# Optimization experiments

Measured on AMD Instinct MI355X. Metric: run time of the kernel, lower is better.

## Reference

```python
import jax, jax.numpy as jnp
import numpy as np

N_NODES = 50000
N_EDGES = 800000
N_GRAPHS = 64
D_IN, D_HID, D_OUT = 128, 128, 64


def setup_inputs() -> dict:
    key = jax.random.key(0)
    ks = jax.random.split(key, 9)
    s = 0.05
    return {
        "x": jax.random.normal(ks[0], (N_NODES, D_IN), jnp.float32),
        "edge_index": jax.random.randint(ks[1], (2, N_EDGES), 0, N_NODES, dtype=jnp.int64),
        "batch": jnp.sort(jax.random.randint(ks[2], (N_NODES,), 0, N_GRAPHS, dtype=jnp.int64)),
        "W1": jax.random.normal(ks[3], (D_IN, D_HID), jnp.float32) * s,
        "b1": jnp.zeros((D_HID,), jnp.float32),
        "W2": jax.random.normal(ks[4], (D_HID, D_HID), jnp.float32) * s,
        "b2": jnp.zeros((D_HID,), jnp.float32),
        "W3": jax.random.normal(ks[5], (D_HID, D_OUT), jnp.float32) * s,
        "b3": jnp.zeros((D_OUT,), jnp.float32),
    }


def _gcn_conv(x, W, b, src, dst, dinv, n_nodes):
    # PyG GCNConv: h = X W; out = sum_{j->i} norm_ij h_j + self-loop term + b
    h = x @ W
    norm_e = dinv[src] * dinv[dst]                      # [E]
    agg = jax.ops.segment_sum(norm_e[:, None] * h[src], dst, num_segments=n_nodes)
    agg = agg + (dinv * dinv)[:, None] * h              # self-loop (norm = dinv_i^2)
    return agg + b


def reference(x, edge_index, batch, W1, b1, W2, b2, W3, b3):
    n_nodes = x.shape[0]
    src, dst = edge_index[0], edge_index[1]
    # symmetric normalization with self-loops: deg_i = in_degree_i + 1
    deg = jax.ops.segment_sum(jnp.ones_like(dst, dtype=x.dtype), dst, num_segments=n_nodes) + 1.0
    dinv = jax.lax.rsqrt(deg)

    h = jax.nn.relu(_gcn_conv(x, W1, b1, src, dst, dinv, n_nodes))
    h = jax.nn.relu(_gcn_conv(h, W2, b2, src, dst, dinv, n_nodes))
    h = _gcn_conv(h, W3, b3, src, dst, dinv, n_nodes)

    # global_mean_pool over graph id
    sums = jax.ops.segment_sum(h, batch, num_segments=N_GRAPHS)
    counts = jax.ops.segment_sum(jnp.ones((n_nodes,), h.dtype), batch, num_segments=N_GRAPHS)
    return sums / jnp.maximum(counts, 1.0)[:, None]
```

## Files before the change

kernel.cpp:

```cpp
#include <hip/hip_runtime.h>

#define NN 50000
#define NE 800000
#define NG 64

typedef short short8 __attribute__((ext_vector_type(8)));
typedef float f32x4 __attribute__((ext_vector_type(4)));

__device__ __forceinline__ unsigned short f2bf(float f) {
    unsigned int u = __float_as_uint(f);
    u = (u + 0x7FFFu + ((u >> 16) & 1u)) >> 16;
    return (unsigned short)u;
}
__device__ __forceinline__ float bf2f(unsigned short h) {
    return __uint_as_float((unsigned int)h << 16);
}

__global__ __launch_bounds__(256) void k_deg(const int* __restrict__ dst, int* __restrict__ degcnt) {
    int e = blockIdx.x * 256 + threadIdx.x;
    if (e < NE) atomicAdd(&degcnt[dst[e]], 1);
}

__global__ __launch_bounds__(256) void k_dinv(const int* __restrict__ degcnt, float* __restrict__ dinv) {
    int i = blockIdx.x * 256 + threadIdx.x;
    if (i < NN) dinv[i] = (float)(1.0 / sqrt((double)degcnt[i] + 1.0));
}

__global__ __launch_bounds__(1024) void k_scan1(const int* __restrict__ cnt, int* __restrict__ row_ptr,
                                                int* __restrict__ blk_sums) {
    __shared__ int s[1024];
    const int tid = threadIdx.x;
    const int i = blockIdx.x * 1024 + tid;
    int v = (i < NN) ? cnt[i] : 0;
    s[tid] = v;
    __syncthreads();
    for (int off = 1; off < 1024; off <<= 1) {
        int t = (tid >= off) ? s[tid - off] : 0;
        __syncthreads();
        s[tid] += t;
        __syncthreads();
    }
    if (i < NN) row_ptr[i] = s[tid] - v;
    if (tid == 1023) blk_sums[blockIdx.x] = s[1023];
}

__global__ __launch_bounds__(64) void k_scan2(int* __restrict__ blk_sums, int nb) {
    int l = threadIdx.x;
    int v = (l < nb) ? blk_sums[l] : 0;
    int incl = v;
    for (int off = 1; off < 64; off <<= 1) {
        int t = __shfl_up(incl, off, 64);
        if (l >= off) incl += t;
    }
    if (l < nb) blk_sums[l] = incl - v;
}

__global__ __launch_bounds__(1024) void k_scan3(int* __restrict__ row_ptr, const int* __restrict__ blk_sums) {
    int i = blockIdx.x * 1024 + threadIdx.x;
    if (i < NN) row_ptr[i] += blk_sums[blockIdx.x];
    if (i == 0) row_ptr[NN] = NE;
}

__global__ __launch_bounds__(256) void k_fill(const int* __restrict__ ei, const int* __restrict__ row_ptr,
                                              int* __restrict__ cursor, int* __restrict__ csr_src) {
    int e = blockIdx.x * 256 + threadIdx.x;
    if (e >= NE) return;
    int s = ei[e];
    int d = ei[NE + e];
    int pos = row_ptr[d] + atomicAdd(&cursor[d], 1);
    csr_src[pos] = s;
}

template <int DO>
__global__ __launch_bounds__(256) void k_gemm_mfma(const float* __restrict__ A, const float* __restrict__ W,
                                                   unsigned short* __restrict__ C, int M) {
    constexpr int NT = DO / 16;
    constexpr int LDK = 136;
    __shared__ __align__(16) unsigned short As[64 * LDK];
    __shared__ __align__(16) unsigned short Wt[DO * LDK];
    const int tid = threadIdx.x;
    const int row0 = blockIdx.x * 64;

    for (int task = tid; task < 64 * (DO / 4); task += 256) {
        const int k0 = (task / (DO / 4)) * 2;
        const int n4 = (task % (DO / 4)) * 4;
        const float4 wa = *(const float4*)&W[(size_t)k0 * DO + n4];
        const float4 wb = *(const float4*)&W[(size_t)(k0 + 1) * DO + n4];
        const float pa[4] = {wa.x, wa.y, wa.z, wa.w};
        const float pb[4] = {wb.x, wb.y, wb.z, wb.w};
#pragma unroll
        for (int i = 0; i < 4; ++i) {
            const unsigned int pk = (unsigned int)f2bf(pa[i]) | ((unsigned int)f2bf(pb[i]) << 16);
            *(unsigned int*)&Wt[(n4 + i) * LDK + k0] = pk;
        }
    }
    {
        const int r = tid >> 2;
        const int ks = (tid & 3) * 32;
        const int grow = row0 + r;
#pragma unroll
        for (int q = 0; q < 8; ++q) {
            float4 v = make_float4(0.f, 0.f, 0.f, 0.f);
            if (grow < M) v = *(const float4*)&A[(size_t)grow * 128 + ks + q * 4];
            const unsigned long long pk =
                (unsigned long long)f2bf(v.x) | ((unsigned long long)f2bf(v.y) << 16) |
                ((unsigned long long)f2bf(v.z) << 32) | ((unsigned long long)f2bf(v.w) << 48);
            *(unsigned long long*)&As[r * LDK + ks + q * 4] = pk;
        }
    }
    __syncthreads();

    const int l = tid & 63;
    const int w = tid >> 6;
    const int lr = l & 15;
    const int lg = l >> 4;
    f32x4 acc[NT];
#pragma unroll
    for (int nt = 0; nt < NT; ++nt) acc[nt] = (f32x4){0.f, 0.f, 0.f, 0.f};

#pragma unroll
    for (int kk = 0; kk < 128; kk += 32) {
        const short8 af = *(const short8*)&As[(w * 16 + lr) * LDK + kk + lg * 8];
#pragma unroll
        for (int nt = 0; nt < NT; ++nt) {
            const short8 bfv = *(const short8*)&Wt[(nt * 16 + lr) * LDK + kk + lg * 8];
            acc[nt] = __builtin_amdgcn_mfma_f32_16x16x32_bf16(af, bfv, acc[nt], 0, 0, 0);
        }
    }

#pragma unroll
    for (int nt = 0; nt < NT; ++nt) {
#pragma unroll
        for (int r = 0; r < 4; ++r) {
            const int grow = row0 + w * 16 + lg * 4 + r;
            if (grow < M) C[(size_t)grow * DO + nt * 16 + lr] = f2bf(acc[nt][r]);
        }
    }
}

template <int D, bool RELU>
__global__ __launch_bounds__(256) void k_agg(const unsigned short* __restrict__ T, const float* __restrict__ bias,
                                             const float* __restrict__ dinv, const int* __restrict__ row_ptr,
                                             const int* __restrict__ csr_src,
                                             float* __restrict__ out) {
    constexpr int G = D / 4;
    constexpr int NPB = 256 / G;
    const int tid = threadIdx.x;
    const int lane = tid % G;
    const int grp = tid / G;
    const int n = blockIdx.x * NPB + grp;
    if (n >= NN) return;

    const float di_n = dinv[n];
    double a0 = 0.0, a1 = 0.0, a2 = 0.0, a3 = 0.0;
    const int beg = row_ptr[n];
    const int end = row_ptr[n + 1];
    int e = beg;
    for (; e + 4 <= end; e += 4) {
        const int s0 = csr_src[e + 0], s1 = csr_src[e + 1], s2 = csr_src[e + 2], s3 = csr_src[e + 3];
        const float w0 = dinv[s0] * di_n, w1 = dinv[s1] * di_n, w2 = dinv[s2] * di_n, w3 = dinv[s3] * di_n;
        const ushort4 v0 = *(const ushort4*)&T[(size_t)s0 * D + lane * 4];
        const ushort4 v1 = *(const ushort4*)&T[(size_t)s1 * D + lane * 4];
        const ushort4 v2 = *(const ushort4*)&T[(size_t)s2 * D + lane * 4];
        const ushort4 v3 = *(const ushort4*)&T[(size_t)s3 * D + lane * 4];
        a0 += (double)w0 * bf2f(v0.x) + (double)w1 * bf2f(v1.x) + (double)w2 * bf2f(v2.x) + (double)w3 * bf2f(v3.x);
        a1 += (double)w0 * bf2f(v0.y) + (double)w1 * bf2f(v1.y) + (double)w2 * bf2f(v2.y) + (double)w3 * bf2f(v3.y);
        a2 += (double)w0 * bf2f(v0.z) + (double)w1 * bf2f(v1.z) + (double)w2 * bf2f(v2.z) + (double)w3 * bf2f(v3.z);
        a3 += (double)w0 * bf2f(v0.w) + (double)w1 * bf2f(v1.w) + (double)w2 * bf2f(v2.w) + (double)w3 * bf2f(v3.w);
    }
    for (; e < end; ++e) {
        const int s = csr_src[e];
        const float w = dinv[s] * di_n;
        const ushort4 v = *(const ushort4*)&T[(size_t)s * D + lane * 4];
        a0 += (double)w * bf2f(v.x);
        a1 += (double)w * bf2f(v.y);
        a2 += (double)w * bf2f(v.z);
        a3 += (double)w * bf2f(v.w);
    }
    {
        const double w = (double)di_n * (double)di_n;
        const ushort4 v = *(const ushort4*)&T[(size_t)n * D + lane * 4];
        a0 += w * bf2f(v.x);
        a1 += w * bf2f(v.y);
        a2 += w * bf2f(v.z);
        a3 += w * bf2f(v.w);
    }
    const float4 b = *(const float4*)&bias[lane * 4];
    a0 += b.x; a1 += b.y; a2 += b.z; a3 += b.w;
    float4 r;
    r.x = (float)a0; r.y = (float)a1; r.z = (float)a2; r.w = (float)a3;
    if (RELU) {
        r.x = fmaxf(r.x, 0.f);
        r.y = fmaxf(r.y, 0.f);
        r.z = fmaxf(r.z, 0.f);
        r.w = fmaxf(r.w, 0.f);
    }
    *(float4*)&out[(size_t)n * D + lane * 4] = r;
}

__global__ __launch_bounds__(256) void k_pool(const float* __restrict__ h, const int* __restrict__ batch,
                                              double* __restrict__ sums, int* __restrict__ cnts) {
    const int NB = 256;
    const int n0 = blockIdx.x * NB;
    const int d = threadIdx.x & 63;
    const int sub = threadIdx.x >> 6;
    double acc = 0.0;
    int cnt = 0;
    int cur = -1;
    for (int i = sub; i < NB; i += 4) {
        int n = n0 + i;
        if (n >= NN) break;
        int g = batch[n];
        if (g != cur) {
            if (cur >= 0) {
                atomicAdd(&sums[cur * 64 + d], acc);
                if (d == 0) atomicAdd(&cnts[cur], cnt);
            }
            cur = g;
            acc = 0.0;
            cnt = 0;
        }
        acc += (double)h[(size_t)n * 64 + d];
        cnt++;
    }
    if (cur >= 0) {
        atomicAdd(&sums[cur * 64 + d], acc);
        if (d == 0) atomicAdd(&cnts[cur], cnt);
    }
}

__global__ __launch_bounds__(256) void k_final(const double* __restrict__ sums, const int* __restrict__ cnts,
                                               float* __restrict__ out) {
    int i = blockIdx.x * 256 + threadIdx.x;
    if (i >= NG * 64) return;
    int g = i >> 6;
    double c = (double)max(cnts[g], 1);
    out[i] = (float)(sums[i] / c);
}

extern "C" void kernel_launch(void* const* d_in, const int* in_sizes, int n_in,
                              void* d_out, int out_size, void* d_ws, size_t ws_size,
                              hipStream_t stream) {
    (void)in_sizes; (void)n_in; (void)out_size; (void)ws_size;
    const float* x     = (const float*)d_in[0];
    const int*   ei    = (const int*)d_in[1];
    const int*   batch = (const int*)d_in[2];
    const float* W1    = (const float*)d_in[3];
    const float* b1    = (const float*)d_in[4];
    const float* W2    = (const float*)d_in[5];
    const float* b2    = (const float*)d_in[6];
    const float* W3    = (const float*)d_in[7];
    const float* b3    = (const float*)d_in[8];
    float* out = (float*)d_out;

    char* w = (char*)d_ws;
    char*  zbase = w;
    int*    degcnt = (int*)w;           w += (size_t)NN * 4;
    int*    cursor = (int*)w;           w += (size_t)NN * 4;
    double* psums  = (double*)w;        w += (size_t)NG * 64 * 8;
    int*    pcnts  = (int*)w;           w += 256;
    size_t zbytes = (size_t)(w - zbase);
    float* dinv     = (float*)w;        w += (size_t)NN * 4;
    int*   row_ptr  = (int*)w;          w += (size_t)(NN + 4) * 4;
    int*   blk_sums = (int*)w;          w += 64 * 4;
    int*   csr_src  = (int*)w;          w += (size_t)NE * 4;
    unsigned short* bufT = (unsigned short*)w;  w += (size_t)NN * 128 * 2;
    float* bufA = (float*)w;            w += (size_t)NN * 128 * 4;

    hipMemsetAsync(zbase, 0, zbytes, stream);

    const int nb_scan = (NN + 1023) / 1024;
    k_deg<<<(NE + 255) / 256, 256, 0, stream>>>(ei + NE, degcnt);
    k_dinv<<<(NN + 255) / 256, 256, 0, stream>>>(degcnt, dinv);
    k_scan1<<<nb_scan, 1024, 0, stream>>>(degcnt, row_ptr, blk_sums);
    k_scan2<<<1, 64, 0, stream>>>(blk_sums, nb_scan);
    k_scan3<<<nb_scan, 1024, 0, stream>>>(row_ptr, blk_sums);
    k_fill<<<(NE + 255) / 256, 256, 0, stream>>>(ei, row_ptr, cursor, csr_src);

    const int gemm_grid = (NN + 63) / 64;
    k_gemm_mfma<128><<<gemm_grid, 256, 0, stream>>>(x, W1, bufT, NN);
    k_agg<128, true><<<(NN + 7) / 8, 256, 0, stream>>>(bufT, b1, dinv, row_ptr, csr_src, bufA);
    k_gemm_mfma<128><<<gemm_grid, 256, 0, stream>>>(bufA, W2, bufT, NN);
    k_agg<128, true><<<(NN + 7) / 8, 256, 0, stream>>>(bufT, b2, dinv, row_ptr, csr_src, bufA);
    k_gemm_mfma<64><<<gemm_grid, 256, 0, stream>>>(bufA, W3, bufT, NN);
    k_agg<64, false><<<(NN + 15) / 16, 256, 0, stream>>>(bufT, b3, dinv, row_ptr, csr_src, bufA);
    k_pool<<<(NN + 255) / 256, 256, 0, stream>>>(bufA, batch, psums, pcnts);
    k_final<<<(NG * 64 + 255) / 256, 256, 0, stream>>>(psums, pcnts, out);
}
```

Before: 297.2 us.

## Build CSR with per-chunk LDS histograms instead of global atomics

Replaces the global atomic degree count and the atomic cursor fill with a two-pass counting sort. Per-chunk shared-memory histograms record each edge's rank within its chunk, and a column scan produces per-chunk offsets, so the fill needs no atomics. The aim is to remove global atomic contention and the zeroed cursor buffer. In exchange it adds two kernels and a 64×50000 uint16 offset table that must be written and read back.

Result: faster. 252.8 us (-14.9%).

```diff
diff --git a/kernel.cpp b/kernel.cpp
--- a/kernel.cpp
+++ b/kernel.cpp
@@ -3,6 +3,9 @@
 #define NN 50000
 #define NE 800000
 #define NG 64
+#define NCHUNK 64
+#define CHUNK 12500
+#define HALF 25000
 
 typedef short short8 __attribute__((ext_vector_type(8)));
 typedef float f32x4 __attribute__((ext_vector_type(4)));
@@ -16,9 +19,41 @@
     return __uint_as_float((unsigned int)h << 16);
 }
 
-__global__ __launch_bounds__(256) void k_deg(const int* __restrict__ dst, int* __restrict__ degcnt) {
-    int e = blockIdx.x * 256 + threadIdx.x;
-    if (e < NE) atomicAdd(&degcnt[dst[e]], 1);
+__global__ __launch_bounds__(1024) void k_hist(const int* __restrict__ ei,
+                                               unsigned short* __restrict__ rank,
+                                               unsigned short* __restrict__ percnt) {
+    __shared__ unsigned int cnt[HALF / 2];
+    const int b = blockIdx.x;
+    const int dbase = blockIdx.y * HALF;
+    const int tid = threadIdx.x;
+    for (int i = tid; i < HALF / 2; i += 1024) cnt[i] = 0;
+    __syncthreads();
+    const int e0 = b * CHUNK;
+    for (int i = tid; i < CHUNK; i += 1024) {
+        const int d = ei[NE + e0 + i];
+        const int local = d - dbase;
+        if ((unsigned)local < (unsigned)HALF) {
+            const unsigned int old = atomicAdd(&cnt[local >> 1], 1u << ((local & 1) * 16));
+            rank[e0 + i] = (unsigned short)((old >> ((local & 1) * 16)) & 0xFFFFu);
+        }
+    }
+    __syncthreads();
+    unsigned int* dst = (unsigned int*)&percnt[(size_t)b * NN + dbase];
+    for (int i = tid; i < HALF / 2; i += 1024) dst[i] = cnt[i];
+}
+
+__global__ __launch_bounds__(256) void k_colscan(unsigned short* __restrict__ percnt,
+                                                 int* __restrict__ degcnt) {
+    const int d = blockIdx.x * 256 + threadIdx.x;
+    if (d >= NN) return;
+    int acc = 0;
+#pragma unroll 8
+    for (int b = 0; b < NCHUNK; ++b) {
+        const int c = percnt[(size_t)b * NN + d];
+        percnt[(size_t)b * NN + d] = (unsigned short)acc;
+        acc += c;
+    }
+    degcnt[d] = acc;
 }
 
 __global__ __launch_bounds__(256) void k_dinv(const int* __restrict__ degcnt, float* __restrict__ dinv) {
@@ -61,13 +96,16 @@
     if (i == 0) row_ptr[NN] = NE;
 }
 
-__global__ __launch_bounds__(256) void k_fill(const int* __restrict__ ei, const int* __restrict__ row_ptr,
-                                              int* __restrict__ cursor, int* __restrict__ csr_src) {
-    int e = blockIdx.x * 256 + threadIdx.x;
+__global__ __launch_bounds__(256) void k_fill3(const int* __restrict__ ei, const int* __restrict__ row_ptr,
+                                               const unsigned short* __restrict__ rank,
+                                               const unsigned short* __restrict__ offs,
+                                               int* __restrict__ csr_src) {
+    const int e = blockIdx.x * 256 + threadIdx.x;
     if (e >= NE) return;
-    int s = ei[e];
-    int d = ei[NE + e];
-    int pos = row_ptr[d] + atomicAdd(&cursor[d], 1);
+    const int s = ei[e];
+    const int d = ei[NE + e];
+    const int b = e / CHUNK;
+    const int pos = row_ptr[d] + (int)offs[(size_t)b * NN + d] + (int)rank[e];
     csr_src[pos] = s;
 }
 
@@ -255,27 +293,29 @@
 
     char* w = (char*)d_ws;
     char*  zbase = w;
-    int*    degcnt = (int*)w;           w += (size_t)NN * 4;
-    int*    cursor = (int*)w;           w += (size_t)NN * 4;
     double* psums  = (double*)w;        w += (size_t)NG * 64 * 8;
     int*    pcnts  = (int*)w;           w += 256;
     size_t zbytes = (size_t)(w - zbase);
-    float* dinv     = (float*)w;        w += (size_t)NN * 4;
-    int*   row_ptr  = (int*)w;          w += (size_t)(NN + 4) * 4;
-    int*   blk_sums = (int*)w;          w += 64 * 4;
-    int*   csr_src  = (int*)w;          w += (size_t)NE * 4;
+    int*    degcnt = (int*)w;           w += (size_t)NN * 4;
+    float*  dinv   = (float*)w;         w += (size_t)NN * 4;
+    int*    row_ptr = (int*)w;          w += (size_t)(NN + 4) * 4;
+    int*    blk_sums = (int*)w;         w += 64 * 4;
+    unsigned short* rank   = (unsigned short*)w;  w += (size_t)NE * 2;
+    unsigned short* percnt = (unsigned short*)w;  w += (size_t)NCHUNK * NN * 2;
+    int*    csr_src = (int*)w;          w += (size_t)NE * 4;
     unsigned short* bufT = (unsigned short*)w;  w += (size_t)NN * 128 * 2;
     float* bufA = (float*)w;            w += (size_t)NN * 128 * 4;
 
     hipMemsetAsync(zbase, 0, zbytes, stream);
 
+    k_hist<<<dim3(NCHUNK, 2), 1024, 0, stream>>>(ei, rank, percnt);
+    k_colscan<<<(NN + 255) / 256, 256, 0, stream>>>(percnt, degcnt);
+    k_dinv<<<(NN + 255) / 256, 256, 0, stream>>>(degcnt, dinv);
     const int nb_scan = (NN + 1023) / 1024;
-    k_deg<<<(NE + 255) / 256, 256, 0, stream>>>(ei + NE, degcnt);
-    k_dinv<<<(NN + 255) / 256, 256, 0, stream>>>(degcnt, dinv);
     k_scan1<<<nb_scan, 1024, 0, stream>>>(degcnt, row_ptr, blk_sums);
     k_scan2<<<1, 64, 0, stream>>>(blk_sums, nb_scan);
     k_scan3<<<nb_scan, 1024, 0, stream>>>(row_ptr, blk_sums);
-    k_fill<<<(NE + 255) / 256, 256, 0, stream>>>(ei, row_ptr, cursor, csr_src);
+    k_fill3<<<(NE + 255) / 256, 256, 0, stream>>>(ei, row_ptr, rank, percnt, csr_src);
 
     const int gemm_grid = (NN + 63) / 64;
     k_gemm_mfma<128><<<gemm_grid, 256, 0, stream>>>(x, W1, bufT, NN);
```
